# Kernel optimization log

Hardware: AMD Instinct MI355X
Metric: run time of the kernel (lower is better)

## Reference

```python
import jax, jax.numpy as jnp
import numpy as np

B, S, QD, KVD = 4, 4096, 512, 512  # batch, seq_len (h*w), q_dim, kv_dim
N_HEAD = 1  # original torch view only works for n_head == 1


def setup_inputs() -> dict:
    key = jax.random.key(0)
    ks = jax.random.split(key, 12)
    s_q = 1.0 / np.sqrt(QD)
    s_kv = 1.0 / np.sqrt(KVD)
    return {
        "x": jax.random.normal(ks[0], (B, S, QD), jnp.float32),
        "y": jax.random.normal(ks[1], (B, S, KVD), jnp.float32),
        # torch nn.Linear weights: (out_features, in_features)
        "Wq": jax.random.normal(ks[2], (QD, QD), jnp.float32) * s_q,
        "bq": jnp.zeros((QD,), jnp.float32),
        "Wqv": jax.random.normal(ks[3], (QD, QD), jnp.float32) * s_q,
        "bqv": jnp.zeros((QD,), jnp.float32),
        "Wk": jax.random.normal(ks[4], (QD, KVD), jnp.float32) * s_kv,
        "bk": jnp.zeros((QD,), jnp.float32),
        "Wkv": jax.random.normal(ks[5], (QD, KVD), jnp.float32) * s_kv,
        "bkv": jnp.zeros((QD,), jnp.float32),
        "Wf": jax.random.normal(ks[6], (QD, QD), jnp.float32) * s_q,
        "bf": jnp.zeros((QD,), jnp.float32),
    }


def _linear(t, W, b):
    return jnp.einsum("bsd,od->bso", t, W) + b


def reference(x, y, Wq, bq, Wqv, bqv, Wk, bk, Wkv, bkv, Wf, bf):
    # projections
    q = _linear(x, Wq, bq)     # [B,S,D] query from target face
    qv = _linear(x, Wqv, bqv)  # [B,S,D] additive value stream from query side
    k = _linear(y, Wk, bk)     # [B,S,D]
    kv = _linear(y, Wkv, bkv)  # [B,S,D]
    # n_head == 1: the (B,S,1,D)->(B,1,S,D) transpose is a no-op reshape,
    # so attend directly over [B,S,D]. NOTE: no 1/sqrt(d) scaling (faithful).
    qk = jnp.einsum("bqd,bkd->bqk", q, k)          # [B,S,S]
    attn = jax.nn.softmax(qk, axis=-1)
    out = jnp.einsum("bqk,bkd->bqd", attn, kv) + qv  # fused AV + qv residual
    return _linear(out, Wf, bf)
```

## Files before the change

kernel.cpp:

```cpp
#include <hip/hip_runtime.h>

typedef _Float16 f16;
typedef _Float16 f16x8 __attribute__((ext_vector_type(8)));
typedef _Float16 f16x4 __attribute__((ext_vector_type(4)));
typedef float    f32x4 __attribute__((ext_vector_type(4)));

#define NB 4
#define SEQ 4096
#define DIM 512
#define MTOT (NB*SEQ)
#define NEL ((size_t)MTOT*DIM)

__global__ __launch_bounds__(256) void proj_gemm(
    const float* __restrict__ x, const float* __restrict__ y,
    const float* __restrict__ Wq, const float* __restrict__ bq,
    const float* __restrict__ Wqv, const float* __restrict__ bqv,
    const float* __restrict__ Wk, const float* __restrict__ bk,
    const float* __restrict__ Wkv, const float* __restrict__ bkv,
    f16* __restrict__ qh, f16* __restrict__ qvh,
    f16* __restrict__ kS, f16* __restrict__ vS)
{
    __shared__ __attribute__((aligned(16))) f16 a_lds[128][40];
    __shared__ __attribute__((aligned(16))) f16 b_lds[128][40];

    const int p = blockIdx.z;
    const float* A    = (p < 2) ? x : y;
    const float* W    = (p==0)?Wq:(p==1)?Wqv:(p==2)?Wk:Wkv;
    const float* bias = (p==0)?bq:(p==1)?bqv:(p==2)?bk:bkv;

    const int m0 = blockIdx.y * 128, n0 = blockIdx.x * 128;
    const int tid = threadIdx.x, lane = tid & 63, wv = tid >> 6;
    const int wm = wv >> 1, wn = wv & 1, mrow = lane & 15, qd = lane >> 4;

    f32x4 acc[4][4];
#pragma unroll
    for (int mt = 0; mt < 4; ++mt)
#pragma unroll
        for (int nt = 0; nt < 4; ++nt) acc[mt][nt] = (f32x4){0.f,0.f,0.f,0.f};

    float bv[4];
#pragma unroll
    for (int nt = 0; nt < 4; ++nt) bv[nt] = bias[n0 + wn*64 + nt*16 + mrow];

    for (int k0 = 0; k0 < DIM; k0 += 32) {
        __syncthreads();
#pragma unroll
        for (int i = 0; i < 4; ++i) {
            int c = i*256 + tid;
            int row = c >> 3, c4 = c & 7;
            float4 v = *(const float4*)(A + (size_t)(m0+row)*DIM + k0 + c4*4);
            f16x4 hh = { (f16)v.x, (f16)v.y, (f16)v.z, (f16)v.w };
            *(f16x4*)&a_lds[row][c4*4] = hh;
        }
#pragma unroll
        for (int i = 0; i < 4; ++i) {
            int c = i*256 + tid;
            int row = c >> 3, c4 = c & 7;
            float4 v = *(const float4*)(W + (size_t)(n0+row)*DIM + k0 + c4*4);
            f16x4 hh = { (f16)v.x, (f16)v.y, (f16)v.z, (f16)v.w };
            *(f16x4*)&b_lds[row][c4*4] = hh;
        }
        __syncthreads();
        f16x8 af[4], bfr[4];
#pragma unroll
        for (int mt = 0; mt < 4; ++mt) af[mt]  = *(const f16x8*)&a_lds[wm*64 + mt*16 + mrow][qd*8];
#pragma unroll
        for (int nt = 0; nt < 4; ++nt) bfr[nt] = *(const f16x8*)&b_lds[wn*64 + nt*16 + mrow][qd*8];
#pragma unroll
        for (int mt = 0; mt < 4; ++mt)
#pragma unroll
            for (int nt = 0; nt < 4; ++nt)
                acc[mt][nt] = __builtin_amdgcn_mfma_f32_16x16x32_f16(af[mt], bfr[nt], acc[mt][nt], 0,0,0);
    }

#pragma unroll
    for (int mt = 0; mt < 4; ++mt)
#pragma unroll
        for (int r = 0; r < 4; ++r) {
            int g = m0 + wm*64 + mt*16 + qd*4 + r;
#pragma unroll
            for (int nt = 0; nt < 4; ++nt) {
                int d = n0 + wn*64 + nt*16 + mrow;
                f16 val = (f16)(acc[mt][nt][r] + bv[nt]);
                if (p == 0) {
                    qh[(size_t)g*DIM + d] = val;
                } else if (p == 1) {
                    qvh[(size_t)g*DIM + d] = val;
                } else if (p == 2) {
                    int b = g >> 12, s = g & 4095;
                    int t = s >> 5, n = s & 31;
                    int chunk = d >> 8, ksl = (d >> 5) & 7, q = (d >> 3) & 3, j = d & 7;
                    size_t idx = (((size_t)((b*128 + t)*2048 + chunk*1024
                                   + n*32 + ((ksl*4 + q + n) & 31))) << 3) + j;
                    kS[idx] = val;
                } else {
                    int b = g >> 12, s = g & 4095;
                    int t = s >> 5, q = (s >> 3) & 3, j = s & 7;
                    int chunk = d >> 8, dl = d & 255;
                    size_t idx = (((size_t)((b*128 + t)*2048 + chunk*1024
                                   + dl*4 + ((q + (dl >> 1)) & 3))) << 3) + j;
                    vS[idx] = val;
                }
            }
        }
}

__device__ __forceinline__ void gl_lds16(const f16* g, f16* l)
{
    __builtin_amdgcn_global_load_lds(
        (const __attribute__((address_space(1))) void*)g,
        (__attribute__((address_space(3))) void*)l, 16, 0, 0);
}

__global__ __launch_bounds__(512, 2) void attn_kernel(
    const f16* __restrict__ qh, const f16* __restrict__ kS,
    const f16* __restrict__ vS, const f16* __restrict__ qvh,
    f16* __restrict__ ao)
{
    __shared__ __attribute__((aligned(16))) f16 kbuf[2][16384];
    __shared__ __attribute__((aligned(16))) f16 vbuf[2][16384];
    __shared__ __attribute__((aligned(16))) float xch[2][4][2][512];

    const int xcd = blockIdx.x & 7;
    const int b   = xcd >> 1;
    const int qt  = (blockIdx.x >> 3) * 2 + (xcd & 1);
    const int tid = threadIdx.x, lane = tid & 63, w = tid >> 6;
    const int qg = w & 3, h = w >> 2;
    const int mrow = lane & 15, qd = lane >> 4;

    const f16* kSb = kS + ((size_t)b << 21);
    const f16* vSb = vS + ((size_t)b << 21);

    const size_t qrow = ((size_t)b*SEQ + qt*64 + qg*16 + mrow) * DIM;
    f16x8 qf[8];
#pragma unroll
    for (int i = 0; i < 8; ++i)
        qf[i] = *(const f16x8*)(qh + qrow + (h*8 + i)*32 + qd*8);

    f32x4 o[16];
#pragma unroll
    for (int nt = 0; nt < 16; ++nt) o[nt] = (f32x4){0.f,0.f,0.f,0.f};
    f32x4 o_l = (f32x4){0.f,0.f,0.f,0.f};
    float m_i[4] = {-INFINITY,-INFINITY,-INFINITY,-INFINITY};
    const f16x8 ones = {(f16)1.f,(f16)1.f,(f16)1.f,(f16)1.f,
                        (f16)1.f,(f16)1.f,(f16)1.f,(f16)1.f};

    const int n0a = mrow, n1a = 16 + mrow;
    const int cbase = h * 1024;

#pragma unroll
    for (int u = 0; u < 4; ++u) {
        const int ub = (u*8 + w) * 64;
        gl_lds16(kSb + (size_t)(ub + lane)*8,        (f16*)&kbuf[0][ub*8]);
    }
#pragma unroll
    for (int u = 0; u < 4; ++u) {
        const int ub = (u*8 + w) * 64;
        gl_lds16(vSb + (size_t)(ub + lane)*8,        (f16*)&vbuf[0][ub*8]);
    }
#pragma unroll
    for (int u = 0; u < 4; ++u) {
        const int ub = (u*8 + w) * 64;
        gl_lds16(kSb + (size_t)(2048 + ub + lane)*8, (f16*)&kbuf[1][ub*8]);
    }
    __syncthreads();

    f32x4 s0p = (f32x4){0.f,0.f,0.f,0.f}, s1p = s0p;
    {
        const f16* kb = &kbuf[0][0];
        __builtin_amdgcn_s_setprio(1);
#pragma unroll
        for (int ksl = 0; ksl < 8; ++ksl) {
            f16x8 kf0 = *(const f16x8*)&kb[(cbase + n0a*32 + ((ksl*4 + qd + n0a) & 31)) << 3];
            f16x8 kf1 = *(const f16x8*)&kb[(cbase + n1a*32 + ((ksl*4 + qd + n1a) & 31)) << 3];
            s0p = __builtin_amdgcn_mfma_f32_16x16x32_f16(qf[ksl], kf0, s0p, 0,0,0);
            s1p = __builtin_amdgcn_mfma_f32_16x16x32_f16(qf[ksl], kf1, s1p, 0,0,0);
        }
        __builtin_amdgcn_s_setprio(0);
        f32x4* slot0 = (f32x4*)&xch[0][qg][h][0];
        slot0[lane]      = s0p;
        slot0[64 + lane] = s1p;
    }
    __syncthreads();

    for (int j = 0; j < 128; ++j) {
        {
            const size_t tk = (size_t)((j + 2) & 127) * 2048;
            const size_t tv = (size_t)((j + 1) & 127) * 2048;
            f16* kd = &kbuf[j & 1][0];
            f16* vd = &vbuf[(j + 1) & 1][0];
#pragma unroll
            for (int u = 0; u < 4; ++u) {
                const int ub = (u*8 + w) * 64;
                gl_lds16(kSb + (tk + ub + lane)*8, kd + ub*8);
                gl_lds16(vSb + (tv + ub + lane)*8, vd + ub*8);
            }
        }

        float* slotr = &xch[j & 1][qg][h ^ 1][0];
        f32x4 s0 = ((const f32x4*)slotr)[lane];
        f32x4 s1 = ((const f32x4*)slotr)[64 + lane];
#pragma unroll
        for (int rr = 0; rr < 4; ++rr) { s0[rr] += s0p[rr]; s1[rr] += s1p[rr]; }

        float pm[4];
        bool need = false;
#pragma unroll
        for (int rr = 0; rr < 4; ++rr) {
            float v = fmaxf(s0[rr], s1[rr]);
            v = fmaxf(v, __shfl_xor(v, 1));
            v = fmaxf(v, __shfl_xor(v, 2));
            v = fmaxf(v, __shfl_xor(v, 4));
            v = fmaxf(v, __shfl_xor(v, 8));
            pm[rr] = v;
            if (v > m_i[rr] + 8.f) need = true;
        }
        if (__any(need)) {
#pragma unroll
            for (int rr = 0; rr < 4; ++rr) {
                float mn = fmaxf(m_i[rr], pm[rr]);
                float alpha = __expf(m_i[rr] - mn);
                m_i[rr] = mn;
#pragma unroll
                for (int nt = 0; nt < 16; ++nt) o[nt][rr] *= alpha;
                o_l[rr] *= alpha;
            }
        }
#pragma unroll
        for (int rr = 0; rr < 4; ++rr) {
            s0[rr] = __expf(s0[rr] - m_i[rr]);
            s1[rr] = __expf(s1[rr] - m_i[rr]);
        }

        f16* pb = (f16*)slotr;
#pragma unroll
        for (int rr = 0; rr < 4; ++rr) {
            pb[(qd*4 + rr)*40 + mrow]      = (f16)s0[rr];
            pb[(qd*4 + rr)*40 + 16 + mrow] = (f16)s1[rr];
        }
        f16x8 pf = *(const f16x8*)&pb[mrow*40 + qd*8];
        o_l = __builtin_amdgcn_mfma_f32_16x16x32_f16(pf, ones, o_l, 0,0,0);

        {
            const f16* vb = &vbuf[j & 1][0];
            __builtin_amdgcn_s_setprio(1);
#pragma unroll
            for (int nt = 0; nt < 16; ++nt) {
                int dl = nt*16 + mrow;
                f16x8 vf = *(const f16x8*)&vb[(cbase + dl*4 + ((qd + (dl >> 1)) & 3)) << 3];
                o[nt] = __builtin_amdgcn_mfma_f32_16x16x32_f16(pf, vf, o[nt], 0,0,0);
            }
            __builtin_amdgcn_s_setprio(0);
        }

        if (j < 127) {
            const f16* kb = &kbuf[(j + 1) & 1][0];
            f32x4 a0 = (f32x4){0.f,0.f,0.f,0.f}, a1 = a0;
            __builtin_amdgcn_s_setprio(1);
#pragma unroll
            for (int ksl = 0; ksl < 8; ++ksl) {
                f16x8 kf0 = *(const f16x8*)&kb[(cbase + n0a*32 + ((ksl*4 + qd + n0a) & 31)) << 3];
                f16x8 kf1 = *(const f16x8*)&kb[(cbase + n1a*32 + ((ksl*4 + qd + n1a) & 31)) << 3];
                a0 = __builtin_amdgcn_mfma_f32_16x16x32_f16(qf[ksl], kf0, a0, 0,0,0);
                a1 = __builtin_amdgcn_mfma_f32_16x16x32_f16(qf[ksl], kf1, a1, 0,0,0);
            }
            __builtin_amdgcn_s_setprio(0);
            s0p = a0; s1p = a1;
            f32x4* slotw = (f32x4*)&xch[(j + 1) & 1][qg][h][0];
            slotw[lane]      = s0p;
            slotw[64 + lane] = s1p;
        }

        __syncthreads();
    }

#pragma unroll
    for (int rr = 0; rr < 4; ++rr) {
        float inv_l = 1.f / o_l[rr];
        size_t grow = ((size_t)b*SEQ + qt*64 + qg*16 + qd*4 + rr) * DIM + h*256;
#pragma unroll
        for (int nt = 0; nt < 16; ++nt) {
            int col = nt*16 + mrow;
            float val = o[nt][rr] * inv_l + (float)qvh[grow + col];
            ao[grow + col] = (f16)val;
        }
    }
}

__global__ __launch_bounds__(256) void final_gemm(
    const f16* __restrict__ ao, const float* __restrict__ Wf,
    const float* __restrict__ bf, float* __restrict__ out)
{
    __shared__ __attribute__((aligned(16))) f16 a_lds[128][40];
    __shared__ __attribute__((aligned(16))) f16 b_lds[128][40];

    const int m0 = blockIdx.y * 128, n0 = blockIdx.x * 128;
    const int tid = threadIdx.x, lane = tid & 63, wv = tid >> 6;
    const int wm = wv >> 1, wn = wv & 1, mrow = lane & 15, qd = lane >> 4;

    f32x4 acc[4][4];
#pragma unroll
    for (int mt = 0; mt < 4; ++mt)
#pragma unroll
        for (int nt = 0; nt < 4; ++nt) acc[mt][nt] = (f32x4){0.f,0.f,0.f,0.f};

    float bv[4];
#pragma unroll
    for (int nt = 0; nt < 4; ++nt) bv[nt] = bf[n0 + wn*64 + nt*16 + mrow];

    for (int k0 = 0; k0 < DIM; k0 += 32) {
        __syncthreads();
#pragma unroll
        for (int i = 0; i < 2; ++i) {
            int c = i*256 + tid;
            int row = c >> 2, c8 = c & 3;
            *(f16x8*)&a_lds[row][c8*8] =
                *(const f16x8*)(ao + (size_t)(m0+row)*DIM + k0 + c8*8);
        }
#pragma unroll
        for (int i = 0; i < 4; ++i) {
            int c = i*256 + tid;
            int row = c >> 3, c4 = c & 7;
            float4 v = *(const float4*)(Wf + (size_t)(n0+row)*DIM + k0 + c4*4);
            f16x4 hh = { (f16)v.x, (f16)v.y, (f16)v.z, (f16)v.w };
            *(f16x4*)&b_lds[row][c4*4] = hh;
        }
        __syncthreads();
        f16x8 af[4], bfr[4];
#pragma unroll
        for (int mt = 0; mt < 4; ++mt) af[mt]  = *(const f16x8*)&a_lds[wm*64 + mt*16 + mrow][qd*8];
#pragma unroll
        for (int nt = 0; nt < 4; ++nt) bfr[nt] = *(const f16x8*)&b_lds[wn*64 + nt*16 + mrow][qd*8];
#pragma unroll
        for (int mt = 0; mt < 4; ++mt)
#pragma unroll
            for (int nt = 0; nt < 4; ++nt)
                acc[mt][nt] = __builtin_amdgcn_mfma_f32_16x16x32_f16(af[mt], bfr[nt], acc[mt][nt], 0,0,0);
    }
#pragma unroll
    for (int mt = 0; mt < 4; ++mt)
#pragma unroll
        for (int r = 0; r < 4; ++r) {
            size_t grow = (size_t)(m0 + wm*64 + mt*16 + qd*4 + r) * DIM;
#pragma unroll
            for (int nt = 0; nt < 4; ++nt) {
                int col = n0 + wn*64 + nt*16 + mrow;
                out[grow + col] = acc[mt][nt][r] + bv[nt];
            }
        }
}

extern "C" void kernel_launch(void* const* d_in, const int* in_sizes, int n_in,
                              void* d_out, int out_size, void* d_ws, size_t ws_size,
                              hipStream_t stream)
{
    const float* x   = (const float*)d_in[0];
    const float* y   = (const float*)d_in[1];
    const float* Wq  = (const float*)d_in[2];
    const float* bq  = (const float*)d_in[3];
    const float* Wqv = (const float*)d_in[4];
    const float* bqv = (const float*)d_in[5];
    const float* Wk  = (const float*)d_in[6];
    const float* bk  = (const float*)d_in[7];
    const float* Wkv = (const float*)d_in[8];
    const float* bkv = (const float*)d_in[9];
    const float* Wf  = (const float*)d_in[10];
    const float* bf  = (const float*)d_in[11];
    float* out = (float*)d_out;

    f16* qh  = (f16*)d_ws;
    f16* qvh = qh  + NEL;
    f16* kS  = qvh + NEL;
    f16* vS  = kS  + NEL;
    f16* aob = vS  + NEL;

    proj_gemm<<<dim3(4, 128, 4), 256, 0, stream>>>(
        x, y, Wq, bq, Wqv, bqv, Wk, bk, Wkv, bkv, qh, qvh, kS, vS);
    attn_kernel<<<dim3(256), 512, 0, stream>>>(qh, kS, vS, qvh, aob);
    final_gemm<<<dim3(4, 128), 256, 0, stream>>>(aob, Wf, bf, out);
}
```

Before: 531.4 us.

## Pre-convert inputs and weights to fp16 and use async LDS loads in GEMMs

Adds a conversion kernel that writes fp16 copies of x, y and all five weight matrices into workspace. New fp16 projection and final GEMM kernels then stage tiles with global_load_lds DMA instead of converting on the fly through registers, which shrinks per-tile load traffic and register work. When the workspace is too small it falls back to the old fp32 path. The attention kernel's s_setprio hints are also removed. The cost is an extra pass over x and y (read fp32, write fp16), and the new LDS layout has no padding, which may cause bank conflicts.

```diff
diff --git a/kernel.cpp b/kernel.cpp
--- a/kernel.cpp
+++ b/kernel.cpp
@@ -10,22 +10,56 @@
 #define DIM 512
 #define MTOT (NB*SEQ)
 #define NEL ((size_t)MTOT*DIM)
-
-__global__ __launch_bounds__(256) void proj_gemm(
+#define WELEM ((size_t)DIM*DIM)
+
+__device__ __forceinline__ void gl_lds16(const f16* g, f16* l)
+{
+    __builtin_amdgcn_global_load_lds(
+        (const __attribute__((address_space(1))) void*)g,
+        (__attribute__((address_space(3))) void*)l, 16, 0, 0);
+}
+
+__global__ __launch_bounds__(256) void convert_kernel(
     const float* __restrict__ x, const float* __restrict__ y,
-    const float* __restrict__ Wq, const float* __restrict__ bq,
-    const float* __restrict__ Wqv, const float* __restrict__ bqv,
-    const float* __restrict__ Wk, const float* __restrict__ bk,
-    const float* __restrict__ Wkv, const float* __restrict__ bkv,
+    const float* __restrict__ Wq, const float* __restrict__ Wqv,
+    const float* __restrict__ Wk, const float* __restrict__ Wkv,
+    const float* __restrict__ Wf,
+    f16* __restrict__ xh, f16* __restrict__ yh, f16* __restrict__ Wh)
+{
+    const size_t q4 = NEL / 4;
+    const size_t w4 = WELEM / 4;
+    const size_t total = 2*q4 + 5*w4;
+    for (size_t u = (size_t)blockIdx.x*blockDim.x + threadIdx.x; u < total;
+         u += (size_t)gridDim.x*blockDim.x) {
+        const float* src; f16* dst; size_t off;
+        if (u < q4)            { src = x;  dst = xh; off = u; }
+        else if (u < 2*q4)     { src = y;  dst = yh; off = u - q4; }
+        else {
+            size_t w = u - 2*q4;
+            int wi = (int)(w / w4); off = w - (size_t)wi*w4;
+            src = (wi==0)?Wq:(wi==1)?Wqv:(wi==2)?Wk:(wi==3)?Wkv:Wf;
+            dst = Wh + (size_t)wi*WELEM;
+        }
+        float4 v = ((const float4*)src)[off];
+        f16x4 h = { (f16)v.x, (f16)v.y, (f16)v.z, (f16)v.w };
+        ((f16x4*)dst)[off] = h;
+    }
+}
+
+__global__ __launch_bounds__(256) void proj_gemm16(
+    const f16* __restrict__ xh, const f16* __restrict__ yh,
+    const f16* __restrict__ Wh,
+    const float* __restrict__ bq, const float* __restrict__ bqv,
+    const float* __restrict__ bk, const float* __restrict__ bkv,
     f16* __restrict__ qh, f16* __restrict__ qvh,
     f16* __restrict__ kS, f16* __restrict__ vS)
 {
-    __shared__ __attribute__((aligned(16))) f16 a_lds[128][40];
-    __shared__ __attribute__((aligned(16))) f16 b_lds[128][40];
+    __shared__ __attribute__((aligned(16))) f16 a_lds[128*32];
+    __shared__ __attribute__((aligned(16))) f16 b_lds[128*32];
 
     const int p = blockIdx.z;
-    const float* A    = (p < 2) ? x : y;
-    const float* W    = (p==0)?Wq:(p==1)?Wqv:(p==2)?Wk:Wkv;
+    const f16* A    = (p < 2) ? xh : yh;
+    const f16* W    = Wh + (size_t)p * WELEM;
     const float* bias = (p==0)?bq:(p==1)?bqv:(p==2)?bk:bkv;
 
     const int m0 = blockIdx.y * 128, n0 = blockIdx.x * 128;
@@ -42,30 +76,24 @@
 #pragma unroll
     for (int nt = 0; nt < 4; ++nt) bv[nt] = bias[n0 + wn*64 + nt*16 + mrow];
 
+    const int srow = lane >> 2, scol = (lane & 3) * 8;
+
     for (int k0 = 0; k0 < DIM; k0 += 32) {
         __syncthreads();
 #pragma unroll
-        for (int i = 0; i < 4; ++i) {
-            int c = i*256 + tid;
-            int row = c >> 3, c4 = c & 7;
-            float4 v = *(const float4*)(A + (size_t)(m0+row)*DIM + k0 + c4*4);
-            f16x4 hh = { (f16)v.x, (f16)v.y, (f16)v.z, (f16)v.w };
-            *(f16x4*)&a_lds[row][c4*4] = hh;
-        }
-#pragma unroll
-        for (int i = 0; i < 4; ++i) {
-            int c = i*256 + tid;
-            int row = c >> 3, c4 = c & 7;
-            float4 v = *(const float4*)(W + (size_t)(n0+row)*DIM + k0 + c4*4);
-            f16x4 hh = { (f16)v.x, (f16)v.y, (f16)v.z, (f16)v.w };
-            *(f16x4*)&b_lds[row][c4*4] = hh;
+        for (int i = 0; i < 2; ++i) {
+            int c = wv*2 + i;
+            gl_lds16(A + (size_t)(m0 + c*16 + srow)*DIM + k0 + scol, &a_lds[c*512]);
+            gl_lds16(W + (size_t)(n0 + c*16 + srow)*DIM + k0 + scol, &b_lds[c*512]);
         }
         __syncthreads();
         f16x8 af[4], bfr[4];
 #pragma unroll
-        for (int mt = 0; mt < 4; ++mt) af[mt]  = *(const f16x8*)&a_lds[wm*64 + mt*16 + mrow][qd*8];
-#pragma unroll
-        for (int nt = 0; nt < 4; ++nt) bfr[nt] = *(const f16x8*)&b_lds[wn*64 + nt*16 + mrow][qd*8];
+        for (int mt = 0; mt < 4; ++mt)
+            af[mt]  = *(const f16x8*)&a_lds[(wm*64 + mt*16 + mrow)*32 + qd*8];
+#pragma unroll
+        for (int nt = 0; nt < 4; ++nt)
+            bfr[nt] = *(const f16x8*)&b_lds[(wn*64 + nt*16 + mrow)*32 + qd*8];
 #pragma unroll
         for (int mt = 0; mt < 4; ++mt)
 #pragma unroll
@@ -105,11 +133,156 @@
         }
 }
 
-__device__ __forceinline__ void gl_lds16(const f16* g, f16* l)
-{
-    __builtin_amdgcn_global_load_lds(
-        (const __attribute__((address_space(1))) void*)g,
-        (__attribute__((address_space(3))) void*)l, 16, 0, 0);
+__global__ __launch_bounds__(256) void final_gemm16(
+    const f16* __restrict__ ao, const f16* __restrict__ Wfh,
+    const float* __restrict__ bf, float* __restrict__ out)
+{
+    __shared__ __attribute__((aligned(16))) f16 a_lds[128*32];
+    __shared__ __attribute__((aligned(16))) f16 b_lds[128*32];
+
+    const int m0 = blockIdx.y * 128, n0 = blockIdx.x * 128;
+    const int tid = threadIdx.x, lane = tid & 63, wv = tid >> 6;
+    const int wm = wv >> 1, wn = wv & 1, mrow = lane & 15, qd = lane >> 4;
+
+    f32x4 acc[4][4];
+#pragma unroll
+    for (int mt = 0; mt < 4; ++mt)
+#pragma unroll
+        for (int nt = 0; nt < 4; ++nt) acc[mt][nt] = (f32x4){0.f,0.f,0.f,0.f};
+
+    float bv[4];
+#pragma unroll
+    for (int nt = 0; nt < 4; ++nt) bv[nt] = bf[n0 + wn*64 + nt*16 + mrow];
+
+    const int srow = lane >> 2, scol = (lane & 3) * 8;
+
+    for (int k0 = 0; k0 < DIM; k0 += 32) {
+        __syncthreads();
+#pragma unroll
+        for (int i = 0; i < 2; ++i) {
+            int c = wv*2 + i;
+            gl_lds16(ao  + (size_t)(m0 + c*16 + srow)*DIM + k0 + scol, &a_lds[c*512]);
+            gl_lds16(Wfh + (size_t)(n0 + c*16 + srow)*DIM + k0 + scol, &b_lds[c*512]);
+        }
+        __syncthreads();
+        f16x8 af[4], bfr[4];
+#pragma unroll
+        for (int mt = 0; mt < 4; ++mt)
+            af[mt]  = *(const f16x8*)&a_lds[(wm*64 + mt*16 + mrow)*32 + qd*8];
+#pragma unroll
+        for (int nt = 0; nt < 4; ++nt)
+            bfr[nt] = *(const f16x8*)&b_lds[(wn*64 + nt*16 + mrow)*32 + qd*8];
+#pragma unroll
+        for (int mt = 0; mt < 4; ++mt)
+#pragma unroll
+            for (int nt = 0; nt < 4; ++nt)
+                acc[mt][nt] = __builtin_amdgcn_mfma_f32_16x16x32_f16(af[mt], bfr[nt], acc[mt][nt], 0,0,0);
+    }
+#pragma unroll
+    for (int mt = 0; mt < 4; ++mt)
+#pragma unroll
+        for (int r = 0; r < 4; ++r) {
+            size_t grow = (size_t)(m0 + wm*64 + mt*16 + qd*4 + r) * DIM;
+#pragma unroll
+            for (int nt = 0; nt < 4; ++nt) {
+                int col = n0 + wn*64 + nt*16 + mrow;
+                out[grow + col] = acc[mt][nt][r] + bv[nt];
+            }
+        }
+}
+
+__global__ __launch_bounds__(256) void proj_gemm(
+    const float* __restrict__ x, const float* __restrict__ y,
+    const float* __restrict__ Wq, const float* __restrict__ bq,
+    const float* __restrict__ Wqv, const float* __restrict__ bqv,
+    const float* __restrict__ Wk, const float* __restrict__ bk,
+    const float* __restrict__ Wkv, const float* __restrict__ bkv,
+    f16* __restrict__ qh, f16* __restrict__ qvh,
+    f16* __restrict__ kS, f16* __restrict__ vS)
+{
+    __shared__ __attribute__((aligned(16))) f16 a_lds[128][40];
+    __shared__ __attribute__((aligned(16))) f16 b_lds[128][40];
+
+    const int p = blockIdx.z;
+    const float* A    = (p < 2) ? x : y;
+    const float* W    = (p==0)?Wq:(p==1)?Wqv:(p==2)?Wk:Wkv;
+    const float* bias = (p==0)?bq:(p==1)?bqv:(p==2)?bk:bkv;
+
+    const int m0 = blockIdx.y * 128, n0 = blockIdx.x * 128;
+    const int tid = threadIdx.x, lane = tid & 63, wv = tid >> 6;
+    const int wm = wv >> 1, wn = wv & 1, mrow = lane & 15, qd = lane >> 4;
+
+    f32x4 acc[4][4];
+#pragma unroll
+    for (int mt = 0; mt < 4; ++mt)
+#pragma unroll
+        for (int nt = 0; nt < 4; ++nt) acc[mt][nt] = (f32x4){0.f,0.f,0.f,0.f};
+
+    float bv[4];
+#pragma unroll
+    for (int nt = 0; nt < 4; ++nt) bv[nt] = bias[n0 + wn*64 + nt*16 + mrow];
+
+    for (int k0 = 0; k0 < DIM; k0 += 32) {
+        __syncthreads();
+#pragma unroll
+        for (int i = 0; i < 4; ++i) {
+            int c = i*256 + tid;
+            int row = c >> 3, c4 = c & 7;
+            float4 v = *(const float4*)(A + (size_t)(m0+row)*DIM + k0 + c4*4);
+            f16x4 hh = { (f16)v.x, (f16)v.y, (f16)v.z, (f16)v.w };
+            *(f16x4*)&a_lds[row][c4*4] = hh;
+        }
+#pragma unroll
+        for (int i = 0; i < 4; ++i) {
+            int c = i*256 + tid;
+            int row = c >> 3, c4 = c & 7;
+            float4 v = *(const float4*)(W + (size_t)(n0+row)*DIM + k0 + c4*4);
+            f16x4 hh = { (f16)v.x, (f16)v.y, (f16)v.z, (f16)v.w };
+            *(f16x4*)&b_lds[row][c4*4] = hh;
+        }
+        __syncthreads();
+        f16x8 af[4], bfr[4];
+#pragma unroll
+        for (int mt = 0; mt < 4; ++mt) af[mt]  = *(const f16x8*)&a_lds[wm*64 + mt*16 + mrow][qd*8];
+#pragma unroll
+        for (int nt = 0; nt < 4; ++nt) bfr[nt] = *(const f16x8*)&b_lds[wn*64 + nt*16 + mrow][qd*8];
+#pragma unroll
+        for (int mt = 0; mt < 4; ++mt)
+#pragma unroll
+            for (int nt = 0; nt < 4; ++nt)
+                acc[mt][nt] = __builtin_amdgcn_mfma_f32_16x16x32_f16(af[mt], bfr[nt], acc[mt][nt], 0,0,0);
+    }
+
+#pragma unroll
+    for (int mt = 0; mt < 4; ++mt)
+#pragma unroll
+        for (int r = 0; r < 4; ++r) {
+            int g = m0 + wm*64 + mt*16 + qd*4 + r;
+#pragma unroll
+            for (int nt = 0; nt < 4; ++nt) {
+                int d = n0 + wn*64 + nt*16 + mrow;
+                f16 val = (f16)(acc[mt][nt][r] + bv[nt]);
+                if (p == 0) {
+                    qh[(size_t)g*DIM + d] = val;
+                } else if (p == 1) {
+                    qvh[(size_t)g*DIM + d] = val;
+                } else if (p == 2) {
+                    int b = g >> 12, s = g & 4095;
+                    int t = s >> 5, n = s & 31;
+                    int chunk = d >> 8, ksl = (d >> 5) & 7, q = (d >> 3) & 3, j = d & 7;
+                    size_t idx = (((size_t)((b*128 + t)*2048 + chunk*1024
+                                   + n*32 + ((ksl*4 + q + n) & 31))) << 3) + j;
+                    kS[idx] = val;
+                } else {
+                    int b = g >> 12, s = g & 4095;
+                    int t = s >> 5, q = (s >> 3) & 3, j = s & 7;
+                    int chunk = d >> 8, dl = d & 255;
+                    size_t idx = (((size_t)((b*128 + t)*2048 + chunk*1024
+                                   + dl*4 + ((q + (dl >> 1)) & 3))) << 3) + j;
+                    vS[idx] = val;
+                }
+            }
+        }
 }
 
 __global__ __launch_bounds__(512, 2) void attn_kernel(
@@ -168,7 +341,6 @@
     f32x4 s0p = (f32x4){0.f,0.f,0.f,0.f}, s1p = s0p;
     {
         const f16* kb = &kbuf[0][0];
-        __builtin_amdgcn_s_setprio(1);
 #pragma unroll
         for (int ksl = 0; ksl < 8; ++ksl) {
             f16x8 kf0 = *(const f16x8*)&kb[(cbase + n0a*32 + ((ksl*4 + qd + n0a) & 31)) << 3];
@@ -176,7 +348,6 @@
             s0p = __builtin_amdgcn_mfma_f32_16x16x32_f16(qf[ksl], kf0, s0p, 0,0,0);
             s1p = __builtin_amdgcn_mfma_f32_16x16x32_f16(qf[ksl], kf1, s1p, 0,0,0);
         }
-        __builtin_amdgcn_s_setprio(0);
         f32x4* slot0 = (f32x4*)&xch[0][qg][h][0];
         slot0[lane]      = s0p;
         slot0[64 + lane] = s1p;
@@ -243,20 +414,17 @@
 
         {
             const f16* vb = &vbuf[j & 1][0];
-            __builtin_amdgcn_s_setprio(1);
 #pragma unroll
             for (int nt = 0; nt < 16; ++nt) {
                 int dl = nt*16 + mrow;
                 f16x8 vf = *(const f16x8*)&vb[(cbase + dl*4 + ((qd + (dl >> 1)) & 3)) << 3];
                 o[nt] = __builtin_amdgcn_mfma_f32_16x16x32_f16(pf, vf, o[nt], 0,0,0);
             }
-            __builtin_amdgcn_s_setprio(0);
         }
 
         if (j < 127) {
             const f16* kb = &kbuf[(j + 1) & 1][0];
             f32x4 a0 = (f32x4){0.f,0.f,0.f,0.f}, a1 = a0;
-            __builtin_amdgcn_s_setprio(1);
 #pragma unroll
             for (int ksl = 0; ksl < 8; ++ksl) {
                 f16x8 kf0 = *(const f16x8*)&kb[(cbase + n0a*32 + ((ksl*4 + qd + n0a) & 31)) << 3];
@@ -264,7 +432,6 @@
                 a0 = __builtin_amdgcn_mfma_f32_16x16x32_f16(qf[ksl], kf0, a0, 0,0,0);
                 a1 = __builtin_amdgcn_mfma_f32_16x16x32_f16(qf[ksl], kf1, a1, 0,0,0);
             }
-            __builtin_amdgcn_s_setprio(0);
             s0p = a0; s1p = a1;
             f32x4* slotw = (f32x4*)&xch[(j + 1) & 1][qg][h][0];
             slotw[lane]      = s0p;
@@ -373,9 +540,27 @@
     f16* kS  = qvh + NEL;
     f16* vS  = kS  + NEL;
     f16* aob = vS  + NEL;
-
-    proj_gemm<<<dim3(4, 128, 4), 256, 0, stream>>>(
-        x, y, Wq, bq, Wqv, bqv, Wk, bk, Wkv, bkv, qh, qvh, kS, vS);
+    f16* xh  = aob + NEL;
+    f16* yh  = xh  + NEL;
+    f16* Wh  = yh  + NEL;
+
+    const size_t need_fast = (7*NEL + 5*WELEM) * sizeof(f16);
+    const bool fast = (ws_size >= need_fast);
+
+    if (fast) {
+        convert_kernel<<<2048, 256, 0, stream>>>(x, y, Wq, Wqv, Wk, Wkv, Wf, xh, yh, Wh);
+        proj_gemm16<<<dim3(4, 128, 4), 256, 0, stream>>>(
+            xh, yh, Wh, bq, bqv, bk, bkv, qh, qvh, kS, vS);
+    } else {
+        proj_gemm<<<dim3(4, 128, 4), 256, 0, stream>>>(
+            x, y, Wq, bq, Wqv, bqv, Wk, bk, Wkv, bkv, qh, qvh, kS, vS);
+    }
+
     attn_kernel<<<dim3(256), 512, 0, stream>>>(qh, kS, vS, qvh, aob);
-    final_gemm<<<dim3(4, 128), 256, 0, stream>>>(aob, Wf, bf, out);
-}
+
+    if (fast) {
+        final_gemm16<<<dim3(4, 128), 256, 0, stream>>>(aob, Wh + 4*WELEM, bf, out);
+    } else {
+        final_gemm<<<dim3(4, 128), 256, 0, stream>>>(aob, Wf, bf, out);
+    }
+}
```

After: 500.0 us. -5.9%, faster.
